# Optimization experiments

Measured on AMD Instinct MI355X. Metric: run time of the kernel, lower is better.

Reference implementation:

```python
import jax, jax.numpy as jnp
import numpy as np

EPS = 1e-9

def _quaternion_normalize(q):
    # normalize last dim with eps for stability
    return q / jnp.sqrt(jnp.sum(q * q, axis=-1, keepdims=True) + EPS)

def setup_inputs() -> dict:
    key = jax.random.key(0)
    k1, k2 = jax.random.split(key)
    # byte trajectory values in [0, 255), float so they carry gradients
    starcoder_bytes = jax.random.uniform(k1, (4096,), dtype=jnp.float32) * 255.0
    # DNA indices 0:A 1:C 2:G 3:T
    hg38_indices = jax.random.randint(k2, (4096,), 0, 4)
    return {"starcoder_bytes": starcoder_bytes, "hg38_indices": hg38_indices}

def _gauss_linking(r1, r2):
    # discrete Gauss linking integral over segment midpoints
    dr1 = r1[1:] - r1[:-1]              # [N-1, 3] segment tangents
    dr2 = r2[1:] - r2[:-1]              # [M-1, 3]
    m1 = 0.5 * (r1[1:] + r1[:-1])       # [N-1, 3] midpoints
    m2 = 0.5 * (r2[1:] + r2[:-1])       # [M-1, 3]
    diff = m1[:, None, :] - m2[None, :, :]            # [N-1, M-1, 3]
    cr = jnp.cross(dr1[:, None, :], dr2[None, :, :])  # [N-1, M-1, 3]
    num = jnp.sum(cr * diff, axis=-1)                 # [N-1, M-1]
    dist2 = jnp.sum(diff * diff, axis=-1) + EPS
    return jnp.sum(num * dist2 ** -1.5) / (4.0 * jnp.pi)

def reference(starcoder_bytes, hg38_indices):
    # map_bytes_to_quaternion
    theta = starcoder_bytes / 255.0 * (2.0 * jnp.pi)
    c, s = jnp.cos(theta), jnp.sin(theta)
    q_algo = _quaternion_normalize(
        jnp.stack([c, 0.5 * s, 0.3 * s, 0.2 * s], axis=-1))  # [N, 4]
    # map_fasta_to_quaternion (one-hot basis, already unit norm)
    basis = jnp.eye(4, dtype=jnp.float32)
    q_bio = _quaternion_normalize(basis[hg38_indices])        # [M, 4]
    # imaginary parts -> 3D trajectories
    r1 = q_algo[:, 1:]
    r2 = q_bio[:, 1:]
    lk = _gauss_linking(r1, r2)
    return lk
```

## Files before the change

### kernel.cpp

```cpp
#include <hip/hip_runtime.h>
#include <math.h>

#define N 4096
#define M 4095
#define EPSF 1e-9f
#define NT 1024
#define INV_4PI 0.07957747154594767f
#define TWO_PI 6.28318530717958647692f

__global__ __launch_bounds__(NT) void fused_gauss_kernel(
    const float* __restrict__ bytes, const int* __restrict__ idx,
    float* __restrict__ out) {
  __shared__ float r1x[N], r1y[N], r1z[N];
  __shared__ int hist[16];
  __shared__ float wsum[NT / 64];

  const int tid = threadIdx.x;
  if (tid < 16) hist[tid] = 0;
  __syncthreads();

#pragma unroll
  for (int k = 0; k < N / NT; ++k) {
    int i = tid + k * NT;
    float b = bytes[i];
    float theta = (b / 255.0f) * TWO_PI;
    float s, c;
    sincosf(theta, &s, &c);
    float q1 = 0.5f * s, q2 = 0.3f * s, q3 = 0.2f * s;
    float n2 = c * c + q1 * q1 + q2 * q2 + q3 * q3 + EPSF;
    float inv = 1.0f / sqrtf(n2);
    r1x[i] = q1 * inv;
    r1y[i] = q2 * inv;
    r1z[i] = q3 * inv;
    if (i < M) {
      int a = idx[i], bb = idx[i + 1];
      if (a != bb) atomicAdd(&hist[a * 4 + bb], 1);
    }
  }
  __syncthreads();

  const float PX[4] = {0.f, 1.f, 0.f, 0.f};
  const float PY[4] = {0.f, 0.f, 1.f, 0.f};
  const float PZ[4] = {0.f, 0.f, 0.f, 1.f};

  float cn[16];
#pragma unroll
  for (int t = 0; t < 16; ++t) cn[t] = (float)hist[t];

  float acc = 0.0f;
#pragma unroll
  for (int k = 0; k < 4; ++k) {
    int i = tid + k * NT;
    if (i < M) {
      float ax = r1x[i], ay = r1y[i], az = r1z[i];
      float bx = r1x[i + 1], by = r1y[i + 1], bz = r1z[i + 1];
      float d1x = bx - ax, d1y = by - ay, d1z = bz - az;
      float m1x = 0.5f * (bx + ax), m1y = 0.5f * (by + ay), m1z = 0.5f * (bz + az);

#pragma unroll
      for (int t = 0; t < 16; ++t) {
        const int a = t >> 2, b = t & 3;
        if (a == b) continue;
        const float ex = PX[b] - PX[a];
        const float ey = PY[b] - PY[a];
        const float ez = PZ[b] - PZ[a];
        const float m2x = 0.5f * (PX[a] + PX[b]);
        const float m2y = 0.5f * (PY[a] + PY[b]);
        const float m2z = 0.5f * (PZ[a] + PZ[b]);

        float dx = m1x - m2x, dy = m1y - m2y, dz = m1z - m2z;
        float cx = d1y * ez - d1z * ey;
        float cy = d1z * ex - d1x * ez;
        float cz = d1x * ey - d1y * ex;
        float num = cx * dx + cy * dy + cz * dz;
        float d2 = dx * dx + dy * dy + dz * dz + EPSF;
        float inv = rsqrtf(d2);
        inv = inv * (1.5f - 0.5f * d2 * inv * inv);
        acc += cn[t] * num * (inv * inv * inv);
      }
    }
  }

  for (int off = 32; off > 0; off >>= 1)
    acc += __shfl_down(acc, off, 64);
  int lane = tid & 63, wid = tid >> 6;
  if (lane == 0) wsum[wid] = acc;
  __syncthreads();
  if (tid == 0) {
    float t = 0.0f;
#pragma unroll
    for (int w = 0; w < NT / 64; ++w) t += wsum[w];
    out[0] = t * INV_4PI;
  }
}

extern "C" void kernel_launch(void* const* d_in, const int* in_sizes, int n_in,
                              void* d_out, int out_size, void* d_ws, size_t ws_size,
                              hipStream_t stream) {
  const float* bytes = (const float*)d_in[0];
  const int* idx = (const int*)d_in[1];
  float* out = (float*)d_out;

  fused_gauss_kernel<<<dim3(1), dim3(NT), 0, stream>>>(bytes, idx, out);
}
```

Baseline: 66.01 us.

## Split single-block kernel across 16 blocks with atomic output accumulation

Replaces the single 1024-thread block with 16 blocks of 256 threads, each handling 256 segments. Every block recomputes the 16-bin transition histogram redundantly, and each thread computes its two trajectory points directly instead of staging them in shared memory. Partial sums are combined with a global atomicAdd after a memset of the output. This spreads the work across more compute units at the cost of redundant histogram work, an extra memset launch, and a nondeterministic floating-point summation order.

```diff
diff --git a/kernel.cpp b/kernel.cpp
--- a/kernel.cpp
+++ b/kernel.cpp
@@ -4,37 +4,37 @@
 #define N 4096
 #define M 4095
 #define EPSF 1e-9f
-#define NT 1024
+#define NB 16
+#define BT 256
 #define INV_4PI 0.07957747154594767f
 #define TWO_PI 6.28318530717958647692f
 
-__global__ __launch_bounds__(NT) void fused_gauss_kernel(
+
+__device__ inline void r1_point(float b, float& x, float& y, float& z) {
+  float theta = (b / 255.0f) * TWO_PI;
+  float s, c;
+  sincosf(theta, &s, &c);
+  float q1 = 0.5f * s, q2 = 0.3f * s, q3 = 0.2f * s;
+  float inv = 1.0f / sqrtf(c * c + q1 * q1 + q2 * q2 + q3 * q3 + EPSF);
+  x = q1 * inv; y = q2 * inv; z = q3 * inv;
+}
+
+__global__ __launch_bounds__(BT) void gauss_kernel(
     const float* __restrict__ bytes, const int* __restrict__ idx,
     float* __restrict__ out) {
-  __shared__ float r1x[N], r1y[N], r1z[N];
   __shared__ int hist[16];
-  __shared__ float wsum[NT / 64];
+  __shared__ float wsum[BT / 64];
 
   const int tid = threadIdx.x;
   if (tid < 16) hist[tid] = 0;
   __syncthreads();
 
 #pragma unroll
-  for (int k = 0; k < N / NT; ++k) {
-    int i = tid + k * NT;
-    float b = bytes[i];
-    float theta = (b / 255.0f) * TWO_PI;
-    float s, c;
-    sincosf(theta, &s, &c);
-    float q1 = 0.5f * s, q2 = 0.3f * s, q3 = 0.2f * s;
-    float n2 = c * c + q1 * q1 + q2 * q2 + q3 * q3 + EPSF;
-    float inv = 1.0f / sqrtf(n2);
-    r1x[i] = q1 * inv;
-    r1y[i] = q2 * inv;
-    r1z[i] = q3 * inv;
-    if (i < M) {
-      int a = idx[i], bb = idx[i + 1];
-      if (a != bb) atomicAdd(&hist[a * 4 + bb], 1);
+  for (int r = 0; r < 16; ++r) {
+    int j = tid + r * BT;
+    if (j < M) {
+      int a = idx[j], b = idx[j + 1];
+      if (a != b) atomicAdd(&hist[a * 4 + b], 1);
     }
   }
   __syncthreads();
@@ -48,36 +48,34 @@
   for (int t = 0; t < 16; ++t) cn[t] = (float)hist[t];
 
   float acc = 0.0f;
-#pragma unroll
-  for (int k = 0; k < 4; ++k) {
-    int i = tid + k * NT;
-    if (i < M) {
-      float ax = r1x[i], ay = r1y[i], az = r1z[i];
-      float bx = r1x[i + 1], by = r1y[i + 1], bz = r1z[i + 1];
-      float d1x = bx - ax, d1y = by - ay, d1z = bz - az;
-      float m1x = 0.5f * (bx + ax), m1y = 0.5f * (by + ay), m1z = 0.5f * (bz + az);
+  int i = blockIdx.x * BT + tid;
+  if (i < M) {
+    float ax, ay, az, bx, by, bz;
+    r1_point(bytes[i], ax, ay, az);
+    r1_point(bytes[i + 1], bx, by, bz);
+    float d1x = bx - ax, d1y = by - ay, d1z = bz - az;
+    float m1x = 0.5f * (bx + ax), m1y = 0.5f * (by + ay), m1z = 0.5f * (bz + az);
 
 #pragma unroll
-      for (int t = 0; t < 16; ++t) {
-        const int a = t >> 2, b = t & 3;
-        if (a == b) continue;
-        const float ex = PX[b] - PX[a];
-        const float ey = PY[b] - PY[a];
-        const float ez = PZ[b] - PZ[a];
-        const float m2x = 0.5f * (PX[a] + PX[b]);
-        const float m2y = 0.5f * (PY[a] + PY[b]);
-        const float m2z = 0.5f * (PZ[a] + PZ[b]);
+    for (int t = 0; t < 16; ++t) {
+      const int a = t >> 2, b = t & 3;
+      if (a == b) continue;
+      const float ex = PX[b] - PX[a];
+      const float ey = PY[b] - PY[a];
+      const float ez = PZ[b] - PZ[a];
+      const float m2x = 0.5f * (PX[a] + PX[b]);
+      const float m2y = 0.5f * (PY[a] + PY[b]);
+      const float m2z = 0.5f * (PZ[a] + PZ[b]);
 
-        float dx = m1x - m2x, dy = m1y - m2y, dz = m1z - m2z;
-        float cx = d1y * ez - d1z * ey;
-        float cy = d1z * ex - d1x * ez;
-        float cz = d1x * ey - d1y * ex;
-        float num = cx * dx + cy * dy + cz * dz;
-        float d2 = dx * dx + dy * dy + dz * dz + EPSF;
-        float inv = rsqrtf(d2);
-        inv = inv * (1.5f - 0.5f * d2 * inv * inv);
-        acc += cn[t] * num * (inv * inv * inv);
-      }
+      float dx = m1x - m2x, dy = m1y - m2y, dz = m1z - m2z;
+      float cx = d1y * ez - d1z * ey;
+      float cy = d1z * ex - d1x * ez;
+      float cz = d1x * ey - d1y * ex;
+      float num = cx * dx + cy * dy + cz * dz;
+      float d2 = dx * dx + dy * dy + dz * dz + EPSF;
+      float inv = rsqrtf(d2);
+      inv = inv * (1.5f - 0.5f * d2 * inv * inv);
+      acc += cn[t] * num * (inv * inv * inv);
     }
   }
 
@@ -87,10 +85,8 @@
   if (lane == 0) wsum[wid] = acc;
   __syncthreads();
   if (tid == 0) {
-    float t = 0.0f;
-#pragma unroll
-    for (int w = 0; w < NT / 64; ++w) t += wsum[w];
-    out[0] = t * INV_4PI;
+    float t = (wsum[0] + wsum[1]) + (wsum[2] + wsum[3]);
+    atomicAdd(out, t * INV_4PI);
   }
 }
 
@@ -101,5 +97,6 @@
   const int* idx = (const int*)d_in[1];
   float* out = (float*)d_out;
 
-  fused_gauss_kernel<<<dim3(1), dim3(NT), 0, stream>>>(bytes, idx, out);
+  hipMemsetAsync(out, 0, sizeof(float), stream);
+  gauss_kernel<<<dim3(NB), dim3(BT), 0, stream>>>(bytes, idx, out);
 }
```

Result: faster. 62.50 us (-5.3%).
